# Kernel optimization log

Measured on AMD Instinct MI355X. Metric: run time of the kernel, lower is better.

Reference implementation:

```python
import jax, jax.numpy as jnp
import numpy as np

Q, C, T, D_IN, D_H = 512, 512, 128, 512, 256


def setup_inputs() -> dict:
    key = jax.random.key(0)
    ks = jax.random.split(key, 8)
    s_in = 1.0 / np.sqrt(D_IN)
    s_h = 1.0 / np.sqrt(D_H)
    return {
        "audio": jax.random.normal(ks[0], (Q, T, D_IN), jnp.float32),
        "video": jax.random.normal(ks[1], (C, T, D_IN), jnp.float32),
        "a_w1": jax.random.normal(ks[2], (D_IN, D_H), jnp.float32) * s_in,
        "a_b1": jnp.zeros((D_H,), jnp.float32),
        "a_w2": jax.random.normal(ks[3], (D_H, D_H), jnp.float32) * s_h,
        "a_b2": jnp.zeros((D_H,), jnp.float32),
        "v_w1": jax.random.normal(ks[4], (D_IN, D_H), jnp.float32) * s_in,
        "v_b1": jnp.zeros((D_H,), jnp.float32),
        "v_w2": jax.random.normal(ks[5], (D_H, D_H), jnp.float32) * s_h,
        "v_b2": jnp.zeros((D_H,), jnp.float32),
        "W": jax.random.normal(ks[6], (D_H, D_H), jnp.float32) * s_h,
        "max_lag": 4,
    }


def _mlp(x, w1, b1, w2, b2):
    # Linear -> ReLU -> Linear
    h = jnp.maximum(x @ w1 + b1, 0.0)
    return h @ w2 + b2


def reference(audio, video, a_w1, a_b1, a_w2, a_b2,
              v_w1, v_b1, v_w2, v_b2, W, max_lag):
    a = _mlp(audio, a_w1, a_b1, a_w2, a_b2)   # [Q, T, D_H]
    v = _mlp(video, v_w1, v_b1, v_w2, v_b2)   # [C, T, D_H]
    # roll along time commutes with the per-frame linear map, so project once
    pv = jnp.einsum('ctd,df->ctf', v, W)      # [C, T, D_H]
    best = None
    for delta in range(-max_lag, max_lag + 1):
        shifted = jnp.roll(pv, delta, axis=1)
        score = jnp.einsum('qtd,ctd->qc', a, shifted)  # [Q, C]
        best = score if best is None else jnp.maximum(best, score)
    return best
```

## Files before the change

kernel.cpp:

```cpp
#include <hip/hip_runtime.h>
#include <cstdint>
#include <cstddef>

typedef __attribute__((ext_vector_type(8))) short frag8;
typedef __attribute__((ext_vector_type(4))) float f32x4;

static __device__ __forceinline__ unsigned short f2bf_r(float f) {
    return (unsigned short)((__float_as_uint(f) + 0x8000u) >> 16);
}

static __device__ __forceinline__ void gll16(const void* g, void* l) {
    __builtin_amdgcn_global_load_lds(
        (const __attribute__((address_space(1))) unsigned int*)g,
        (__attribute__((address_space(3))) unsigned int*)l, 16, 0, 0);
}

__global__ __launch_bounds__(256, 2)
void mlp_fused(const float* __restrict__ X0, const float* __restrict__ X1,
               const unsigned short* __restrict__ W1T0, const unsigned short* __restrict__ W1T1,
               const float* __restrict__ b1v0, const float* __restrict__ b1v1,
               const unsigned short* __restrict__ W2T0, const unsigned short* __restrict__ W2T1,
               const float* __restrict__ b2v0, const float* __restrict__ b2v1,
               unsigned short* __restrict__ O0, unsigned short* __restrict__ O1)
{
    __shared__ __align__(16) unsigned short As[64 * 72];
    __shared__ __align__(16) unsigned short Bs[256 * 64];
    __shared__ __align__(16) unsigned short hs[64 * 264];

    const int mod = blockIdx.y;
    const float* X = mod ? X1 : X0;
    const unsigned short* W1T = mod ? W1T1 : W1T0;
    const unsigned short* W2T = mod ? W2T1 : W2T0;
    const float* b1 = mod ? b1v1 : b1v0;
    const float* b2 = mod ? b2v1 : b2v0;
    unsigned short* O = mod ? O1 : O0;

    const int t    = threadIdx.x;
    const int wave = t >> 6;
    const int lane = t & 63;
    const int quad = lane >> 4;
    const int l15  = lane & 15;
    const int m0   = blockIdx.x * 64;

    const int rowB = lane >> 3;
    const int qB   = (lane & 7) ^ rowB;
    const int nRowBase = wave * 64 + rowB;
    unsigned short* BsW = Bs + wave * 4096;
    const int swz = l15 & 7;

    f32x4 acc[4][4];
    #pragma unroll
    for (int i = 0; i < 4; ++i)
        #pragma unroll
        for (int j = 0; j < 4; ++j)
            acc[i][j] = (f32x4){0.f, 0.f, 0.f, 0.f};

    for (int k0 = 0; k0 < 512; k0 += 64) {
        #pragma unroll
        for (int p = 0; p < 4; ++p) {
            const int idx = p * 256 + t;
            const int row = idx >> 4;
            const int col = (idx & 15) * 4;
            const float4 v = *(const float4*)(X + (size_t)(m0 + row) * 512 + k0 + col);
            const unsigned int a0 = __float_as_uint(v.x) + 0x8000u;
            const unsigned int a1 = __float_as_uint(v.y) + 0x8000u;
            const unsigned int a2 = __float_as_uint(v.z) + 0x8000u;
            const unsigned int a3 = __float_as_uint(v.w) + 0x8000u;
            uint2 pk;
            pk.x = __builtin_amdgcn_perm(a1, a0, 0x07060302u);
            pk.y = __builtin_amdgcn_perm(a3, a2, 0x07060302u);
            *(uint2*)&As[row * 72 + col] = pk;
        }
        #pragma unroll
        for (int p = 0; p < 8; ++p)
            gll16(W1T + (size_t)(nRowBase + p * 8) * 512 + qB * 8 + k0, BsW + p * 512);
        __syncthreads();

        frag8 af[2][4], bf[2][4];
        #pragma unroll
        for (int i = 0; i < 4; ++i)
            #pragma unroll
            for (int kh = 0; kh < 2; ++kh)
                af[kh][i] = *(const frag8*)&As[(i * 16 + l15) * 72 + kh * 32 + quad * 8];
        #pragma unroll
        for (int j = 0; j < 4; ++j) {
            const int row = wave * 64 + j * 16 + l15;
            #pragma unroll
            for (int kh = 0; kh < 2; ++kh)
                bf[kh][j] = *(const frag8*)&Bs[row * 64 + (((kh * 4 + quad) ^ swz) * 8)];
        }
        #pragma unroll
        for (int kh = 0; kh < 2; ++kh)
            #pragma unroll
            for (int i = 0; i < 4; ++i)
                #pragma unroll
                for (int j = 0; j < 4; ++j)
                    acc[i][j] = __builtin_amdgcn_mfma_f32_16x16x32_bf16(af[kh][i], bf[kh][j], acc[i][j], 0, 0, 0);
        __syncthreads();
    }

    #pragma unroll
    for (int j = 0; j < 4; ++j) {
        const int col = wave * 64 + j * 16 + l15;
        const float bv = b1[col];
        #pragma unroll
        for (int i = 0; i < 4; ++i) {
            const int rl = i * 16 + quad * 4;
            #pragma unroll
            for (int r = 0; r < 4; ++r)
                hs[(rl + r) * 264 + col] = f2bf_r(fmaxf(acc[i][j][r] + bv, 0.0f));
        }
    }
    __syncthreads();

    #pragma unroll
    for (int i = 0; i < 4; ++i)
        #pragma unroll
        for (int j = 0; j < 4; ++j)
            acc[i][j] = (f32x4){0.f, 0.f, 0.f, 0.f};

    for (int k0 = 0; k0 < 256; k0 += 64) {
        #pragma unroll
        for (int p = 0; p < 8; ++p)
            gll16(W2T + (size_t)(nRowBase + p * 8) * 256 + qB * 8 + k0, BsW + p * 512);
        __syncthreads();

        frag8 af[2][4], bf[2][4];
        #pragma unroll
        for (int i = 0; i < 4; ++i)
            #pragma unroll
            for (int kh = 0; kh < 2; ++kh)
                af[kh][i] = *(const frag8*)&hs[(i * 16 + l15) * 264 + k0 + kh * 32 + quad * 8];
        #pragma unroll
        for (int j = 0; j < 4; ++j) {
            const int row = wave * 64 + j * 16 + l15;
            #pragma unroll
            for (int kh = 0; kh < 2; ++kh)
                bf[kh][j] = *(const frag8*)&Bs[row * 64 + (((kh * 4 + quad) ^ swz) * 8)];
        }
        #pragma unroll
        for (int kh = 0; kh < 2; ++kh)
            #pragma unroll
            for (int i = 0; i < 4; ++i)
                #pragma unroll
                for (int j = 0; j < 4; ++j)
                    acc[i][j] = __builtin_amdgcn_mfma_f32_16x16x32_bf16(af[kh][i], bf[kh][j], acc[i][j], 0, 0, 0);
        __syncthreads();
    }

    #pragma unroll
    for (int j = 0; j < 4; ++j) {
        const int col = wave * 64 + j * 16 + l15;
        const float bv = b2[col];
        #pragma unroll
        for (int i = 0; i < 4; ++i) {
            const int rl = i * 16 + quad * 4;
            #pragma unroll
            for (int r = 0; r < 4; ++r)
                hs[(rl + r) * 264 + col] = f2bf_r(acc[i][j][r] + bv);
        }
    }
    __syncthreads();
    #pragma unroll
    for (int u = 0; u < 8; ++u) {
        const int chunk = u * 256 + t;
        const int row = chunk >> 5;
        const int c16 = (chunk & 31) * 8;
        uint4 v = *(const uint4*)&hs[row * 264 + c16];
        *(uint4*)&O[(size_t)(m0 + row) * 256 + c16] = v;
    }
}

__global__ __launch_bounds__(256, 2)
void gemm_corr(const unsigned short* __restrict__ A, const unsigned short* __restrict__ B,
               float* __restrict__ partial)
{
    __shared__ __align__(16) unsigned short As[128 * 64];
    __shared__ __align__(16) unsigned short Bs[128 * 64];

    const int t    = threadIdx.x;
    const int wave = t >> 6;
    const int lane = t & 63;
    const int quad = lane >> 4;
    const int l15  = lane & 15;
    const int wm   = (wave >> 1) * 64;
    const int wn   = (wave & 1) * 64;
    const int m0   = blockIdx.y * 128;
    const int n0   = blockIdx.x * 128;

    const int z      = blockIdx.z;
    const int kStart = (z & 3) * 8192;
    const int delta  = (z >> 2) - 4;
    const int koff   = (32768 - 256 * delta) & 32767;

    const int rowL = (wave << 5) + (lane >> 3);
    const int qL   = (lane & 7) ^ ((lane >> 3) & 7);
    const size_t aBase = (size_t)(m0 + rowL) * 32768 + qL * 8;
    const size_t bBase = (size_t)(n0 + rowL) * 32768 + qL * 8;
    unsigned short* AsW = As + wave * 2048;
    unsigned short* BsW = Bs + wave * 2048;
    const int swz = l15 & 7;

    f32x4 acc[4][4];
    #pragma unroll
    for (int i = 0; i < 4; ++i)
        #pragma unroll
        for (int j = 0; j < 4; ++j)
            acc[i][j] = (f32x4){0.f, 0.f, 0.f, 0.f};

    for (int k0 = 0; k0 < 8192; k0 += 64) {
        const int kA = kStart + k0;
        const int kB = (kA + koff) & 32767;
        #pragma unroll
        for (int p = 0; p < 4; ++p) {
            gll16(A + aBase + (size_t)(p * 8) * 32768 + kA, AsW + p * 512);
            gll16(B + bBase + (size_t)(p * 8) * 32768 + kB, BsW + p * 512);
        }
        __syncthreads();

        frag8 af[2][4], bf[2][4];
        #pragma unroll
        for (int i = 0; i < 4; ++i) {
            const int row = wm + i * 16 + l15;
            #pragma unroll
            for (int kh = 0; kh < 2; ++kh)
                af[kh][i] = *(const frag8*)&As[row * 64 + (((kh * 4 + quad) ^ swz) * 8)];
        }
        #pragma unroll
        for (int j = 0; j < 4; ++j) {
            const int row = wn + j * 16 + l15;
            #pragma unroll
            for (int kh = 0; kh < 2; ++kh)
                bf[kh][j] = *(const frag8*)&Bs[row * 64 + (((kh * 4 + quad) ^ swz) * 8)];
        }
        #pragma unroll
        for (int kh = 0; kh < 2; ++kh)
            #pragma unroll
            for (int i = 0; i < 4; ++i)
                #pragma unroll
                for (int j = 0; j < 4; ++j)
                    acc[i][j] = __builtin_amdgcn_mfma_f32_16x16x32_bf16(af[kh][i], bf[kh][j], acc[i][j], 0, 0, 0);
        __syncthreads();
    }

    float* C = partial + (size_t)z * 262144;
    #pragma unroll
    for (int i = 0; i < 4; ++i) {
        const int rg = m0 + wm + i * 16 + quad * 4;
        #pragma unroll
        for (int j = 0; j < 4; ++j) {
            const int cg = n0 + wn + j * 16 + l15;
            #pragma unroll
            for (int r = 0; r < 4; ++r)
                C[(size_t)(rg + r) * 512 + cg] = acc[i][j][r];
        }
    }
}

__global__ void prep(const float* __restrict__ a_w1, const float* __restrict__ v_w1,
                     const float* __restrict__ a_w2, const float* __restrict__ v_w2,
                     const float* __restrict__ W, const float* __restrict__ v_b2,
                     unsigned short* __restrict__ aw1T, unsigned short* __restrict__ vw1T,
                     unsigned short* __restrict__ aw2T,
                     unsigned short* __restrict__ WcT, float* __restrict__ bc)
{
    const int b = blockIdx.x;
    __shared__ float tl[32][33];
    __shared__ float wcol[256];
    if (b < 320) {
        const float* src; unsigned short* dst; int R, C, tile;
        if (b < 128)      { src = a_w1; dst = aw1T; R = 512; C = 256; tile = b; }
        else if (b < 256) { src = v_w1; dst = vw1T; R = 512; C = 256; tile = b - 128; }
        else              { src = a_w2; dst = aw2T; R = 256; C = 256; tile = b - 256; }
        const int tilesX = C / 32;
        const int bx = (tile % tilesX) * 32, by = (tile / tilesX) * 32;
        const int tx = threadIdx.x & 31, ty = threadIdx.x >> 5;
        #pragma unroll
        for (int r = ty; r < 32; r += 8)
            tl[r][tx] = src[(size_t)(by + r) * C + bx + tx];
        __syncthreads();
        #pragma unroll
        for (int c = ty; c < 32; c += 8)
            dst[(size_t)(bx + c) * R + by + tx] = f2bf_r(tl[tx][c]);
    } else {
        const int n = b - 320, k = threadIdx.x;
        wcol[k] = W[(size_t)k * 256 + n];
        __syncthreads();
        float s = 0.f;
        #pragma unroll 8
        for (int d = 0; d < 256; ++d) s += v_w2[(size_t)k * 256 + d] * wcol[d];
        WcT[(size_t)n * 256 + k] = f2bf_r(s);
        if (k == 0) {
            float tt = 0.f;
            for (int d = 0; d < 256; ++d) tt += v_b2[d] * wcol[d];
            bc[n] = tt;
        }
    }
}

__global__ void reduce_max9(const float* __restrict__ partial, float* __restrict__ out) {
    const int idx = blockIdx.x * blockDim.x + threadIdx.x;
    float best = -3.4e38f;
    #pragma unroll
    for (int dz = 0; dz < 9; ++dz) {
        float s = 0.f;
        #pragma unroll
        for (int ks = 0; ks < 4; ++ks)
            s += partial[((size_t)(dz * 4 + ks) << 18) + idx];
        best = fmaxf(best, s);
    }
    out[idx] = best;
}

extern "C" void kernel_launch(void* const* d_in, const int* in_sizes, int n_in,
                              void* d_out, int out_size, void* d_ws, size_t ws_size,
                              hipStream_t stream) {
    const float* audio = (const float*)d_in[0];
    const float* video = (const float*)d_in[1];
    const float* a_w1  = (const float*)d_in[2];
    const float* a_b1  = (const float*)d_in[3];
    const float* a_w2  = (const float*)d_in[4];
    const float* a_b2  = (const float*)d_in[5];
    const float* v_w1  = (const float*)d_in[6];
    const float* v_b1  = (const float*)d_in[7];
    const float* v_w2  = (const float*)d_in[8];
    const float* v_b2  = (const float*)d_in[9];
    const float* Wm    = (const float*)d_in[10];

    char* ws = (char*)d_ws;
    unsigned short* aw1T = (unsigned short*)(ws + 0);
    unsigned short* vw1T = (unsigned short*)(ws + 262144);
    unsigned short* aw2T = (unsigned short*)(ws + 524288);
    unsigned short* WcT  = (unsigned short*)(ws + 655360);
    float*          bc   = (float*)(ws + 786432);
    unsigned short* a_bf = (unsigned short*)(ws + 1048576);
    unsigned short* pv   = (unsigned short*)(ws + 34603008);
    float* partial       = (float*)(ws + 68157440);
    float* out = (float*)d_out;

    prep<<<dim3(576), 256, 0, stream>>>(a_w1, v_w1, a_w2, v_w2, Wm, v_b2,
                                        aw1T, vw1T, aw2T, WcT, bc);
    mlp_fused<<<dim3(1024, 2), 256, 0, stream>>>(
        audio, video, aw1T, vw1T, a_b1, v_b1, aw2T, WcT, a_b2, bc, a_bf, pv);
    gemm_corr<<<dim3(4, 4, 36), 256, 0, stream>>>(a_bf, pv, partial);
    reduce_max9<<<dim3(1024), 256, 0, stream>>>(partial, out);
}
```

Measured before the change: 499.7 us.

## Rebalance correlation GEMM across lags and load MLP weights straight to registers

The correlation GEMM moves from a fixed (tile, lag, k-split) grid to a stream-K-like split. Each block walks a contiguous run of 144 k-steps across the flattened lag×K space, using 128-wide K tiles with XOR-swizzled LDS. It writes up to two partial segments, and the reduction kernel sums matching segments per lag before taking the max. The fused MLP kernel drops the LDS staging of weight tiles and reads B fragments directly from global memory. It also prefetches the next X tile into registers and raises the occupancy hint to 3 blocks. These changes aim at better load balance, fewer barriers and more overlap, at the cost of a larger partial buffer (64 slices), more global traffic for the weights, and register pressure.

Result: no change. 500.3 us (+0.1%).

```diff
diff --git a/kernel.cpp b/kernel.cpp
--- a/kernel.cpp
+++ b/kernel.cpp
@@ -15,7 +15,7 @@
         (__attribute__((address_space(3))) unsigned int*)l, 16, 0, 0);
 }
 
-__global__ __launch_bounds__(256, 2)
+__global__ __launch_bounds__(256, 3)
 void mlp_fused(const float* __restrict__ X0, const float* __restrict__ X1,
                const unsigned short* __restrict__ W1T0, const unsigned short* __restrict__ W1T1,
                const float* __restrict__ b1v0, const float* __restrict__ b1v1,
@@ -24,7 +24,6 @@
                unsigned short* __restrict__ O0, unsigned short* __restrict__ O1)
 {
     __shared__ __align__(16) unsigned short As[64 * 72];
-    __shared__ __align__(16) unsigned short Bs[256 * 64];
     __shared__ __align__(16) unsigned short hs[64 * 264];
 
     const int mod = blockIdx.y;
@@ -40,13 +39,16 @@
     const int lane = t & 63;
     const int quad = lane >> 4;
     const int l15  = lane & 15;
+    const int wn   = wave * 64;
     const int m0   = blockIdx.x * 64;
 
-    const int rowB = lane >> 3;
-    const int qB   = (lane & 7) ^ rowB;
-    const int nRowBase = wave * 64 + rowB;
-    unsigned short* BsW = Bs + wave * 4096;
-    const int swz = l15 & 7;
+    int xrow[4], xcol[4];
+    #pragma unroll
+    for (int p = 0; p < 4; ++p) {
+        const int idx = p * 256 + t;
+        xrow[p] = idx >> 4;
+        xcol[p] = (idx & 15) * 4;
+    }
 
     f32x4 acc[4][4];
     #pragma unroll
@@ -55,40 +57,42 @@
         for (int j = 0; j < 4; ++j)
             acc[i][j] = (f32x4){0.f, 0.f, 0.f, 0.f};
 
+    float4 xv[4];
+    #pragma unroll
+    for (int p = 0; p < 4; ++p)
+        xv[p] = *(const float4*)(X + (size_t)(m0 + xrow[p]) * 512 + xcol[p]);
+
     for (int k0 = 0; k0 < 512; k0 += 64) {
+        frag8 bf[2][4];
+        #pragma unroll
+        for (int kh = 0; kh < 2; ++kh)
+            #pragma unroll
+            for (int j = 0; j < 4; ++j)
+                bf[kh][j] = *(const frag8*)(W1T + (size_t)(wn + j * 16 + l15) * 512 + k0 + kh * 32 + quad * 8);
         #pragma unroll
         for (int p = 0; p < 4; ++p) {
-            const int idx = p * 256 + t;
-            const int row = idx >> 4;
-            const int col = (idx & 15) * 4;
-            const float4 v = *(const float4*)(X + (size_t)(m0 + row) * 512 + k0 + col);
-            const unsigned int a0 = __float_as_uint(v.x) + 0x8000u;
-            const unsigned int a1 = __float_as_uint(v.y) + 0x8000u;
-            const unsigned int a2 = __float_as_uint(v.z) + 0x8000u;
-            const unsigned int a3 = __float_as_uint(v.w) + 0x8000u;
+            const unsigned int a0 = __float_as_uint(xv[p].x) + 0x8000u;
+            const unsigned int a1 = __float_as_uint(xv[p].y) + 0x8000u;
+            const unsigned int a2 = __float_as_uint(xv[p].z) + 0x8000u;
+            const unsigned int a3 = __float_as_uint(xv[p].w) + 0x8000u;
             uint2 pk;
             pk.x = __builtin_amdgcn_perm(a1, a0, 0x07060302u);
             pk.y = __builtin_amdgcn_perm(a3, a2, 0x07060302u);
-            *(uint2*)&As[row * 72 + col] = pk;
-        }
-        #pragma unroll
-        for (int p = 0; p < 8; ++p)
-            gll16(W1T + (size_t)(nRowBase + p * 8) * 512 + qB * 8 + k0, BsW + p * 512);
+            *(uint2*)&As[xrow[p] * 72 + xcol[p]] = pk;
+        }
+        if (k0 < 448) {
+            #pragma unroll
+            for (int p = 0; p < 4; ++p)
+                xv[p] = *(const float4*)(X + (size_t)(m0 + xrow[p]) * 512 + (k0 + 64) + xcol[p]);
+        }
         __syncthreads();
 
-        frag8 af[2][4], bf[2][4];
+        frag8 af[2][4];
         #pragma unroll
         for (int i = 0; i < 4; ++i)
             #pragma unroll
             for (int kh = 0; kh < 2; ++kh)
                 af[kh][i] = *(const frag8*)&As[(i * 16 + l15) * 72 + kh * 32 + quad * 8];
-        #pragma unroll
-        for (int j = 0; j < 4; ++j) {
-            const int row = wave * 64 + j * 16 + l15;
-            #pragma unroll
-            for (int kh = 0; kh < 2; ++kh)
-                bf[kh][j] = *(const frag8*)&Bs[row * 64 + (((kh * 4 + quad) ^ swz) * 8)];
-        }
         #pragma unroll
         for (int kh = 0; kh < 2; ++kh)
             #pragma unroll
@@ -101,7 +105,7 @@
 
     #pragma unroll
     for (int j = 0; j < 4; ++j) {
-        const int col = wave * 64 + j * 16 + l15;
+        const int col = wn + j * 16 + l15;
         const float bv = b1[col];
         #pragma unroll
         for (int i = 0; i < 4; ++i) {
@@ -119,38 +123,32 @@
         for (int j = 0; j < 4; ++j)
             acc[i][j] = (f32x4){0.f, 0.f, 0.f, 0.f};
 
+    #pragma unroll
     for (int k0 = 0; k0 < 256; k0 += 64) {
-        #pragma unroll
-        for (int p = 0; p < 8; ++p)
-            gll16(W2T + (size_t)(nRowBase + p * 8) * 256 + qB * 8 + k0, BsW + p * 512);
-        __syncthreads();
-
-        frag8 af[2][4], bf[2][4];
+        frag8 bf[2][4], af[2][4];
+        #pragma unroll
+        for (int kh = 0; kh < 2; ++kh)
+            #pragma unroll
+            for (int j = 0; j < 4; ++j)
+                bf[kh][j] = *(const frag8*)(W2T + (size_t)(wn + j * 16 + l15) * 256 + k0 + kh * 32 + quad * 8);
         #pragma unroll
         for (int i = 0; i < 4; ++i)
             #pragma unroll
             for (int kh = 0; kh < 2; ++kh)
                 af[kh][i] = *(const frag8*)&hs[(i * 16 + l15) * 264 + k0 + kh * 32 + quad * 8];
         #pragma unroll
-        for (int j = 0; j < 4; ++j) {
-            const int row = wave * 64 + j * 16 + l15;
-            #pragma unroll
-            for (int kh = 0; kh < 2; ++kh)
-                bf[kh][j] = *(const frag8*)&Bs[row * 64 + (((kh * 4 + quad) ^ swz) * 8)];
-        }
-        #pragma unroll
         for (int kh = 0; kh < 2; ++kh)
             #pragma unroll
             for (int i = 0; i < 4; ++i)
                 #pragma unroll
                 for (int j = 0; j < 4; ++j)
                     acc[i][j] = __builtin_amdgcn_mfma_f32_16x16x32_bf16(af[kh][i], bf[kh][j], acc[i][j], 0, 0, 0);
-        __syncthreads();
-    }
+    }
+    __syncthreads();
 
     #pragma unroll
     for (int j = 0; j < 4; ++j) {
-        const int col = wave * 64 + j * 16 + l15;
+        const int col = wn + j * 16 + l15;
         const float bv = b2[col];
         #pragma unroll
         for (int i = 0; i < 4; ++i) {
@@ -175,8 +173,8 @@
 void gemm_corr(const unsigned short* __restrict__ A, const unsigned short* __restrict__ B,
                float* __restrict__ partial)
 {
-    __shared__ __align__(16) unsigned short As[128 * 64];
-    __shared__ __align__(16) unsigned short Bs[128 * 64];
+    __shared__ __align__(16) unsigned short As[128 * 128];
+    __shared__ __align__(16) unsigned short Bs[128 * 128];
 
     const int t    = threadIdx.x;
     const int wave = t >> 6;
@@ -185,21 +183,15 @@
     const int l15  = lane & 15;
     const int wm   = (wave >> 1) * 64;
     const int wn   = (wave & 1) * 64;
-    const int m0   = blockIdx.y * 128;
-    const int n0   = blockIdx.x * 128;
-
-    const int z      = blockIdx.z;
-    const int kStart = (z & 3) * 8192;
-    const int delta  = (z >> 2) - 4;
-    const int koff   = (32768 - 256 * delta) & 32767;
-
-    const int rowL = (wave << 5) + (lane >> 3);
-    const int qL   = (lane & 7) ^ ((lane >> 3) & 7);
-    const size_t aBase = (size_t)(m0 + rowL) * 32768 + qL * 8;
-    const size_t bBase = (size_t)(n0 + rowL) * 32768 + qL * 8;
-    unsigned short* AsW = As + wave * 2048;
-    unsigned short* BsW = Bs + wave * 2048;
-    const int swz = l15 & 7;
+    const int tile = blockIdx.y;
+    const int m0   = (tile >> 2) * 128;
+    const int n0   = (tile & 3) * 128;
+    const int c    = blockIdx.x;
+
+    const int rloc = lane >> 4;
+    const int g    = lane & 15;
+    const unsigned short* Abase = A + (size_t)m0 * 32768;
+    const unsigned short* Bbase = B + (size_t)n0 * 32768;
 
     f32x4 acc[4][4];
     #pragma unroll
@@ -208,51 +200,66 @@
         for (int j = 0; j < 4; ++j)
             acc[i][j] = (f32x4){0.f, 0.f, 0.f, 0.f};
 
-    for (int k0 = 0; k0 < 8192; k0 += 64) {
-        const int kA = kStart + k0;
-        const int kB = (kA + koff) & 32767;
-        #pragma unroll
-        for (int p = 0; p < 4; ++p) {
-            gll16(A + aBase + (size_t)(p * 8) * 32768 + kA, AsW + p * 512);
-            gll16(B + bBase + (size_t)(p * 8) * 32768 + kB, BsW + p * 512);
-        }
-        __syncthreads();
-
-        frag8 af[2][4], bf[2][4];
+    int seg = 0;
+    int s = c * 144;
+    const int s1 = s + 144;
+    while (s < s1) {
+        const int d    = s >> 9;
+        const int send = min(s1, (d + 1) << 9);
+        const int koff = (32768 - 256 * (d - 4)) & 32767;
+        for (; s < send; s += 2) {
+            const int kA = (s & 511) << 6;
+            const int kB = (kA + koff) & 32767;
+            #pragma unroll
+            for (int p = 0; p < 8; ++p) {
+                const int rlo = p * 4 + rloc;
+                const int sc  = ((g ^ (rlo & 15)) << 3);
+                const int row = wave * 32 + rlo;
+                gll16(Abase + (size_t)row * 32768 + kA + sc, &As[(wave * 32 + p * 4) * 128]);
+                gll16(Bbase + (size_t)row * 32768 + kB + sc, &Bs[(wave * 32 + p * 4) * 128]);
+            }
+            __syncthreads();
+
+            #pragma unroll
+            for (int kh = 0; kh < 4; ++kh) {
+                frag8 af[4], bf[4];
+                #pragma unroll
+                for (int i = 0; i < 4; ++i) {
+                    const int q = (kh * 4 + quad) ^ l15;
+                    af[i] = *(const frag8*)&As[(wm + i * 16 + l15) * 128 + (q << 3)];
+                }
+                #pragma unroll
+                for (int j = 0; j < 4; ++j) {
+                    const int q = (kh * 4 + quad) ^ l15;
+                    bf[j] = *(const frag8*)&Bs[(wn + j * 16 + l15) * 128 + (q << 3)];
+                }
+                #pragma unroll
+                for (int i = 0; i < 4; ++i)
+                    #pragma unroll
+                    for (int j = 0; j < 4; ++j)
+                        acc[i][j] = __builtin_amdgcn_mfma_f32_16x16x32_bf16(af[i], bf[j], acc[i][j], 0, 0, 0);
+            }
+            __syncthreads();
+        }
+        float* C = partial + (size_t)(2 * c + seg) * 262144;
         #pragma unroll
         for (int i = 0; i < 4; ++i) {
-            const int row = wm + i * 16 + l15;
-            #pragma unroll
-            for (int kh = 0; kh < 2; ++kh)
-                af[kh][i] = *(const frag8*)&As[row * 64 + (((kh * 4 + quad) ^ swz) * 8)];
-        }
-        #pragma unroll
-        for (int j = 0; j < 4; ++j) {
-            const int row = wn + j * 16 + l15;
-            #pragma unroll
-            for (int kh = 0; kh < 2; ++kh)
-                bf[kh][j] = *(const frag8*)&Bs[row * 64 + (((kh * 4 + quad) ^ swz) * 8)];
-        }
-        #pragma unroll
-        for (int kh = 0; kh < 2; ++kh)
+            const int rg = m0 + wm + i * 16 + quad * 4;
+            #pragma unroll
+            for (int j = 0; j < 4; ++j) {
+                const int cg = n0 + wn + j * 16 + l15;
+                #pragma unroll
+                for (int r = 0; r < 4; ++r)
+                    C[(size_t)(rg + r) * 512 + cg] = acc[i][j][r];
+            }
+        }
+        ++seg;
+        if (s < s1) {
             #pragma unroll
             for (int i = 0; i < 4; ++i)
                 #pragma unroll
                 for (int j = 0; j < 4; ++j)
-                    acc[i][j] = __builtin_amdgcn_mfma_f32_16x16x32_bf16(af[kh][i], bf[kh][j], acc[i][j], 0, 0, 0);
-        __syncthreads();
-    }
-
-    float* C = partial + (size_t)z * 262144;
-    #pragma unroll
-    for (int i = 0; i < 4; ++i) {
-        const int rg = m0 + wm + i * 16 + quad * 4;
-        #pragma unroll
-        for (int j = 0; j < 4; ++j) {
-            const int cg = n0 + wn + j * 16 + l15;
-            #pragma unroll
-            for (int r = 0; r < 4; ++r)
-                C[(size_t)(rg + r) * 512 + cg] = acc[i][j][r];
+                    acc[i][j] = (f32x4){0.f, 0.f, 0.f, 0.f};
         }
     }
 }
@@ -298,15 +305,19 @@
     }
 }
 
-__global__ void reduce_max9(const float* __restrict__ partial, float* __restrict__ out) {
+__global__ void reduce_lag(const float* __restrict__ partial, float* __restrict__ out) {
     const int idx = blockIdx.x * blockDim.x + threadIdx.x;
     float best = -3.4e38f;
     #pragma unroll
-    for (int dz = 0; dz < 9; ++dz) {
+    for (int d = 0; d < 9; ++d) {
         float s = 0.f;
-        #pragma unroll
-        for (int ks = 0; ks < 4; ++ks)
-            s += partial[((size_t)(dz * 4 + ks) << 18) + idx];
+        const int sb = d << 9, se = sb + 512;
+        #pragma unroll 5
+        for (int c = sb / 144; c * 144 < se; ++c) {
+            const int d0 = (c * 144) >> 9;
+            const int seg = (d0 == d) ? 0 : 1;
+            s += partial[(size_t)(2 * c + seg) * 262144 + idx];
+        }
         best = fmaxf(best, s);
     }
     out[idx] = best;
@@ -342,6 +353,6 @@
                                         aw1T, vw1T, aw2T, WcT, bc);
     mlp_fused<<<dim3(1024, 2), 256, 0, stream>>>(
         audio, video, aw1T, vw1T, a_b1, v_b1, aw2T, WcT, a_b2, bc, a_bf, pv);
-    gemm_corr<<<dim3(4, 4, 36), 256, 0, stream>>>(a_bf, pv, partial);
-    reduce_max9<<<dim3(1024), 256, 0, stream>>>(partial, out);
-}
+    gemm_corr<<<dim3(32, 16), 256, 0, stream>>>(a_bf, pv, partial);
+    reduce_lag<<<dim3(1024), 256, 0, stream>>>(partial, out);
+}
```
